# Performance work log

Hardware: AMD Instinct MI355X
Metric: run time of the kernel (lower is better)

The kernel has to match this reference:

```python
import jax, jax.numpy as jnp
import numpy as np

N = 100000      # nodes
E = 1600000     # edges (avg degree 16)
D_IN, H, D_OUT = 128, 64, 40


def setup_inputs() -> dict:
    key = jax.random.key(0)
    k = jax.random.split(key, 6)
    x = jax.random.normal(k[0], (N, D_IN), dtype=jnp.float32)
    edge_index = jax.random.randint(k[1], (2, E), 0, N, dtype=jnp.int32)
    W1 = jax.random.normal(k[2], (D_IN, H), dtype=jnp.float32) / np.sqrt(D_IN)
    b1 = jnp.zeros((H,), dtype=jnp.float32)
    W2 = jax.random.normal(k[3], (H, D_OUT), dtype=jnp.float32) / np.sqrt(H)
    b2 = jnp.zeros((D_OUT,), dtype=jnp.float32)
    return {"x": x, "edge_index": edge_index, "W1": W1, "b1": b1, "W2": W2, "b2": b2}


def _gcn_conv(h, src, dst, dinv, W, b):
    # PyG GCNConv: linear transform, then D^-1/2 (A+I) D^-1/2 aggregation, then bias.
    h = h @ W                                   # [N, F]
    w = dinv[src] * dinv[dst]                   # [E] symmetric norm edge weights
    msg = h[src] * w[:, None]                   # [E, F] gather + scale
    agg = jax.ops.segment_sum(msg, dst, num_segments=N)  # scatter-add to dst
    agg = agg + h * (dinv * dinv)[:, None]      # self-loop contribution deg^-1 * h
    return agg + b


def reference(x, edge_index, W1, b1, W2, b2):
    src, dst = edge_index[0], edge_index[1]
    # degree with self-loops (in-degree at dst, source_to_target flow)
    deg = 1.0 + jax.ops.segment_sum(jnp.ones((E,), dtype=x.dtype), dst, num_segments=N)
    dinv = jax.lax.rsqrt(deg)
    # dropout (p=0.6) is identity in eval mode
    h = jax.nn.relu(_gcn_conv(x, src, dst, dinv, W1, b1))
    out = _gcn_conv(h, src, dst, dinv, W2, b2)
    return jax.nn.log_softmax(out, axis=1)
```

## Files before the change

### kernel.cpp

```cpp
#include <hip/hip_runtime.h>
#include <math.h>

#define D_IN  128
#define H_DIM 64
#define D_OUT 40
#define BW_SHIFT 9
#define BW_NODES 512
#define BINA_CHUNK 4096
#define BUCKET_CAP 9216

typedef unsigned int uint32;

__device__ __forceinline__ unsigned short f2bf(float v) {
    uint32 b = __float_as_uint(v);
    b += 0x7fffu + ((b >> 16) & 1u);
    return (unsigned short)(b >> 16);
}
__device__ __forceinline__ float bf2f(unsigned short u) {
    return __uint_as_float(((uint32)u) << 16);
}

__global__ void cursor_init_kernel(int* __restrict__ gcursor, int NBUCK) {
    int i = blockIdx.x * 256 + threadIdx.x;
    if (i < NBUCK) gcursor[i] = i * BUCKET_CAP;
}

__global__ __launch_bounds__(256) void binA_scatter_kernel(const int* __restrict__ src,
                                                           const int* __restrict__ dst,
                                                           int* __restrict__ gcursor,
                                                           uint32* __restrict__ binned,
                                                           int E, int NBUCK) {
    __shared__ int cnt[1024];
    __shared__ int lbase[1024];
    int t = threadIdx.x;
    for (int i = t; i < NBUCK; i += 256) cnt[i] = 0;
    __syncthreads();
    int e0 = blockIdx.x * BINA_CHUNK;
    int e1 = min(e0 + BINA_CHUNK, E);
    for (int e = e0 + t; e < e1; e += 256)
        atomicAdd(&cnt[dst[e] >> BW_SHIFT], 1);
    __syncthreads();
    for (int i = t; i < NBUCK; i += 256) {
        int c = cnt[i];
        lbase[i] = c ? atomicAdd(&gcursor[i], c) : 0;
        cnt[i] = 0;
    }
    __syncthreads();
    for (int e = e0 + t; e < e1; e += 256) {
        int d = dst[e];
        int bk = d >> BW_SHIFT;
        int p = lbase[bk] + atomicAdd(&cnt[bk], 1);
        binned[p] = (((uint32)(d & (BW_NODES - 1))) << 23) | (uint32)src[e];
    }
}

__global__ __launch_bounds__(256) void phaseB_kernel(uint32* __restrict__ binned,
                                                     const int* __restrict__ gcur_end,
                                                     int* __restrict__ rows,
                                                     float* __restrict__ dinv,
                                                     int N) {
    __shared__ uint32 sedge[BUCKET_CAP];
    __shared__ int deg[BW_NODES];
    __shared__ int sa[BW_NODES], sb[BW_NODES];
    __shared__ int cur[BW_NODES];
    int b = blockIdx.x;
    int node0 = b << BW_SHIFT;
    int nn = min(BW_NODES, N - node0);
    int base = b * BUCKET_CAP;
    int cnt = gcur_end[b] - base;
    int t = threadIdx.x;
    deg[t] = 0; deg[t + 256] = 0;
    __syncthreads();
    for (int e = t; e < cnt; e += 256) {
        uint32 v = binned[base + e];
        sedge[e] = v;
        atomicAdd(&deg[v >> 23], 1);
    }
    __syncthreads();
    for (int i = t; i < nn; i += 256)
        dinv[node0 + i] = rsqrtf(1.0f + (float)deg[i]);
    sa[t] = deg[t]; sa[t + 256] = deg[t + 256];
    __syncthreads();
    int* pa = sa; int* pb = sb;
    for (int off = 1; off < BW_NODES; off <<= 1) {
        for (int i = t; i < BW_NODES; i += 256)
            pb[i] = pa[i] + ((i >= off) ? pa[i - off] : 0);
        __syncthreads();
        int* tmp = pa; pa = pb; pb = tmp;
    }
    for (int i = t; i < BW_NODES; i += 256)
        cur[i] = (i ? pa[i - 1] : 0);
    __syncthreads();
    int* rb = rows + b * 513;
    for (int i = t; i < nn; i += 256)
        rb[i] = base + cur[i];
    if (t == 0) rb[nn] = base + cnt;
    __syncthreads();
    for (int e = t; e < cnt; e += 256) {
        uint32 v = sedge[e];
        int doff = v >> 23;
        int p = base + atomicAdd(&cur[doff], 1);
        binned[p] = v & 0x7FFFFFu;
    }
}

__global__ __launch_bounds__(256) void gemm1_tn4(const float* __restrict__ x,
                                                 const float* __restrict__ W1,
                                                 const float* __restrict__ dinv,
                                                 unsigned short* __restrict__ h1s, int N) {
    __shared__ float sW[D_IN * H_DIM];
    int t = threadIdx.x;
    for (int i = t; i < D_IN * H_DIM / 4; i += 256)
        reinterpret_cast<float4*>(sW)[i] = reinterpret_cast<const float4*>(W1)[i];
    __syncthreads();

    int n = blockIdx.x * 64 + (t >> 2);
    if (n >= N) return;
    int c0 = (t & 3) * 16;
    const float4* xr = reinterpret_cast<const float4*>(x + (size_t)n * D_IN);

    float acc[16] = {};
    for (int k0 = 0; k0 < D_IN / 4; ++k0) {
        float4 xv = xr[k0];
        #pragma unroll
        for (int kk = 0; kk < 4; ++kk) {
            float xk = (kk == 0) ? xv.x : (kk == 1) ? xv.y : (kk == 2) ? xv.z : xv.w;
            const float* wrow = &sW[(4 * k0 + kk) * H_DIM + c0];
            #pragma unroll
            for (int c = 0; c < 4; ++c) {
                float4 wv = *reinterpret_cast<const float4*>(wrow + 4 * c);
                acc[4 * c + 0] += xk * wv.x;
                acc[4 * c + 1] += xk * wv.y;
                acc[4 * c + 2] += xk * wv.z;
                acc[4 * c + 3] += xk * wv.w;
            }
        }
    }
    float di = dinv[n];
    unsigned short* orow = h1s + (size_t)n * H_DIM + c0;
    #pragma unroll
    for (int c = 0; c < 4; ++c) {
        ushort4 u;
        u.x = f2bf(acc[4 * c + 0] * di);
        u.y = f2bf(acc[4 * c + 1] * di);
        u.z = f2bf(acc[4 * c + 2] * di);
        u.w = f2bf(acc[4 * c + 3] * di);
        *reinterpret_cast<ushort4*>(orow + 4 * c) = u;
    }
}

__global__ __launch_bounds__(256) void agg1_v3(const int* __restrict__ rows,
                                               const int* __restrict__ csr,
                                               const unsigned short* __restrict__ h1s,
                                               const float* __restrict__ dinv,
                                               const float* __restrict__ b1,
                                               float* __restrict__ z, int N) {
    int node = blockIdx.x * 4 + (threadIdx.x >> 6);
    if (node >= N) return;
    int lane = threadIdx.x & 63;
    int e  = lane >> 4;
    int fl = (lane & 15) * 4;
    int ridx = node + (node >> BW_SHIFT);
    int s0 = __builtin_amdgcn_readfirstlane(rows[ridx]);
    int s1 = __builtin_amdgcn_readfirstlane(rows[ridx + 1]);

    float4 acc = make_float4(0.f, 0.f, 0.f, 0.f);
    for (int base = s0; base < s1; base += 64) {
        int cnt = min(64, s1 - base);
        int myc = (lane < cnt) ? csr[base + lane] : 0;
        int j = 0;
        for (; j + 8 <= cnt; j += 8) {
            uint32 sa = (uint32)__shfl(myc, j + e);
            uint32 sb = (uint32)__shfl(myc, j + 4 + e);
            ushort4 ha = *reinterpret_cast<const ushort4*>(h1s + (size_t)(sa * H_DIM + fl));
            ushort4 hb = *reinterpret_cast<const ushort4*>(h1s + (size_t)(sb * H_DIM + fl));
            acc.x += bf2f(ha.x) + bf2f(hb.x);
            acc.y += bf2f(ha.y) + bf2f(hb.y);
            acc.z += bf2f(ha.z) + bf2f(hb.z);
            acc.w += bf2f(ha.w) + bf2f(hb.w);
        }
        for (; j < cnt; j += 4) {
            int idx = j + e;
            uint32 sa = (uint32)__shfl(myc, min(idx, cnt - 1));
            if (idx < cnt) {
                ushort4 hv = *reinterpret_cast<const ushort4*>(h1s + (size_t)(sa * H_DIM + fl));
                acc.x += bf2f(hv.x); acc.y += bf2f(hv.y);
                acc.z += bf2f(hv.z); acc.w += bf2f(hv.w);
            }
        }
    }
    acc.x += __shfl_xor(acc.x, 16); acc.y += __shfl_xor(acc.y, 16);
    acc.z += __shfl_xor(acc.z, 16); acc.w += __shfl_xor(acc.w, 16);
    acc.x += __shfl_xor(acc.x, 32); acc.y += __shfl_xor(acc.y, 32);
    acc.z += __shfl_xor(acc.z, 32); acc.w += __shfl_xor(acc.w, 32);

    if (e == 0) {
        ushort4 sv = *reinterpret_cast<const ushort4*>(h1s + (size_t)node * H_DIM + fl);
        float4 bv = *reinterpret_cast<const float4*>(b1 + fl);
        float di = dinv[node];
        float4 o;
        o.x = fmaxf(0.f, di * (acc.x + bf2f(sv.x)) + bv.x);
        o.y = fmaxf(0.f, di * (acc.y + bf2f(sv.y)) + bv.y);
        o.z = fmaxf(0.f, di * (acc.z + bf2f(sv.z)) + bv.z);
        o.w = fmaxf(0.f, di * (acc.w + bf2f(sv.w)) + bv.w);
        *reinterpret_cast<float4*>(z + (size_t)node * H_DIM + fl) = o;
    }
}

__global__ __launch_bounds__(256) void gemm2_tn2(const float* __restrict__ z,
                                                 const float* __restrict__ W2,
                                                 const float* __restrict__ dinv,
                                                 unsigned short* __restrict__ h2s, int N) {
    __shared__ float sW[H_DIM * D_OUT];
    int t = threadIdx.x;
    for (int i = t; i < H_DIM * D_OUT / 4; i += 256)
        reinterpret_cast<float4*>(sW)[i] = reinterpret_cast<const float4*>(W2)[i];
    __syncthreads();

    int n = blockIdx.x * 128 + (t >> 1);
    if (n >= N) return;
    int c0 = (t & 1) * 20;
    const float4* zr = reinterpret_cast<const float4*>(z + (size_t)n * H_DIM);

    float acc[20] = {};
    for (int k0 = 0; k0 < H_DIM / 4; ++k0) {
        float4 zv = zr[k0];
        #pragma unroll
        for (int kk = 0; kk < 4; ++kk) {
            float zk = (kk == 0) ? zv.x : (kk == 1) ? zv.y : (kk == 2) ? zv.z : zv.w;
            const float* wrow = &sW[(4 * k0 + kk) * D_OUT + c0];
            #pragma unroll
            for (int c = 0; c < 5; ++c) {
                float4 wv = *reinterpret_cast<const float4*>(wrow + 4 * c);
                acc[4 * c + 0] += zk * wv.x;
                acc[4 * c + 1] += zk * wv.y;
                acc[4 * c + 2] += zk * wv.z;
                acc[4 * c + 3] += zk * wv.w;
            }
        }
    }
    float di = dinv[n];
    unsigned short* orow = h2s + (size_t)n * D_OUT + c0;
    #pragma unroll
    for (int c = 0; c < 5; ++c) {
        ushort4 u;
        u.x = f2bf(acc[4 * c + 0] * di);
        u.y = f2bf(acc[4 * c + 1] * di);
        u.z = f2bf(acc[4 * c + 2] * di);
        u.w = f2bf(acc[4 * c + 3] * di);
        *reinterpret_cast<ushort4*>(orow + 4 * c) = u;
    }
}

__global__ __launch_bounds__(256) void agg2_v4(const int* __restrict__ rows,
                                               const int* __restrict__ csr,
                                               const unsigned short* __restrict__ h2s,
                                               const float* __restrict__ dinv,
                                               const float* __restrict__ b2,
                                               float* __restrict__ out, int N) {
    int node = blockIdx.x * 4 + (threadIdx.x >> 6);
    if (node >= N) return;
    int lane = threadIdx.x & 63;
    int g   = lane / 10;
    int f10 = lane - g * 10;
    int fl  = f10 * 4;
    bool gact = g < 6;
    int ridx = node + (node >> BW_SHIFT);
    int s0 = __builtin_amdgcn_readfirstlane(rows[ridx]);
    int s1 = __builtin_amdgcn_readfirstlane(rows[ridx + 1]);

    float4 acc = make_float4(0.f, 0.f, 0.f, 0.f);
    for (int base = s0; base < s1; base += 64) {
        int cnt = min(64, s1 - base);
        int myc = (lane < cnt) ? csr[base + lane] : 0;
        int j = 0;
        for (; j + 12 <= cnt; j += 12) {
            uint32 sa = (uint32)__shfl(myc, min(j + g, 63));
            uint32 sb = (uint32)__shfl(myc, min(j + 6 + g, 63));
            if (gact) {
                ushort4 ha = *reinterpret_cast<const ushort4*>(h2s + (size_t)(sa * D_OUT + fl));
                ushort4 hb = *reinterpret_cast<const ushort4*>(h2s + (size_t)(sb * D_OUT + fl));
                acc.x += bf2f(ha.x) + bf2f(hb.x);
                acc.y += bf2f(ha.y) + bf2f(hb.y);
                acc.z += bf2f(ha.z) + bf2f(hb.z);
                acc.w += bf2f(ha.w) + bf2f(hb.w);
            }
        }
        for (; j < cnt; j += 6) {
            int idx = j + g;
            uint32 sa = (uint32)__shfl(myc, min(idx, cnt - 1));
            if (gact && idx < cnt) {
                ushort4 hv = *reinterpret_cast<const ushort4*>(h2s + (size_t)(sa * D_OUT + fl));
                acc.x += bf2f(hv.x); acc.y += bf2f(hv.y);
                acc.z += bf2f(hv.z); acc.w += bf2f(hv.w);
            }
        }
    }
    acc.x += __shfl(acc.x, min(lane + 30, 63));
    acc.y += __shfl(acc.y, min(lane + 30, 63));
    acc.z += __shfl(acc.z, min(lane + 30, 63));
    acc.w += __shfl(acc.w, min(lane + 30, 63));
    acc.x += __shfl(acc.x, min(lane + 10, 63)) + __shfl(acc.x, min(lane + 20, 63));
    acc.y += __shfl(acc.y, min(lane + 10, 63)) + __shfl(acc.y, min(lane + 20, 63));
    acc.z += __shfl(acc.z, min(lane + 10, 63)) + __shfl(acc.z, min(lane + 20, 63));
    acc.w += __shfl(acc.w, min(lane + 10, 63)) + __shfl(acc.w, min(lane + 20, 63));

    bool act = lane < 10;
    float v0 = -INFINITY, v1 = -INFINITY, v2 = -INFINITY, v3 = -INFINITY;
    if (act) {
        ushort4 sv = *reinterpret_cast<const ushort4*>(h2s + (size_t)node * D_OUT + fl);
        float4 bv = *reinterpret_cast<const float4*>(b2 + fl);
        float di = dinv[node];
        v0 = di * (acc.x + bf2f(sv.x)) + bv.x;
        v1 = di * (acc.y + bf2f(sv.y)) + bv.y;
        v2 = di * (acc.z + bf2f(sv.z)) + bv.z;
        v3 = di * (acc.w + bf2f(sv.w)) + bv.w;
    }
    float mm = act ? fmaxf(fmaxf(v0, v1), fmaxf(v2, v3)) : -INFINITY;
    for (int off = 32; off > 0; off >>= 1) mm = fmaxf(mm, __shfl_xor(mm, off));
    float es = act ? (__expf(v0 - mm) + __expf(v1 - mm) + __expf(v2 - mm) + __expf(v3 - mm)) : 0.f;
    for (int off = 32; off > 0; off >>= 1) es += __shfl_xor(es, off);
    float lse = __logf(es);
    if (act) {
        float4 o = make_float4(v0 - mm - lse, v1 - mm - lse, v2 - mm - lse, v3 - mm - lse);
        *reinterpret_cast<float4*>(out + (size_t)node * D_OUT + fl) = o;
    }
}

extern "C" void kernel_launch(void* const* d_in, const int* in_sizes, int n_in,
                              void* d_out, int out_size, void* d_ws, size_t ws_size,
                              hipStream_t stream) {
    const float* x  = (const float*)d_in[0];
    const int*   ei = (const int*)d_in[1];
    const float* W1 = (const float*)d_in[2];
    const float* b1 = (const float*)d_in[3];
    const float* W2 = (const float*)d_in[4];
    const float* b2 = (const float*)d_in[5];
    float* out = (float*)d_out;

    int N = in_sizes[0] / D_IN;
    int E = in_sizes[1] / 2;
    const int* src = ei;
    const int* dst = ei + E;
    int NBUCK = (N + BW_NODES - 1) / BW_NODES;

    char* p = (char*)d_ws;
    int*   gcursor = (int*)p;  p += 4096;
    int*   rows    = (int*)p;  p += ((size_t)NBUCK * 513 + 64) * 4;
    float* dinv    = (float*)p; p += (((size_t)N + 63) & ~(size_t)63) * 4;
    uint32* binned = (uint32*)p; p += (size_t)NBUCK * BUCKET_CAP * 4;
    unsigned short* h1s = (unsigned short*)p; p += (size_t)N * H_DIM * 2;
    float* z       = (float*)p; p += (size_t)N * H_DIM * 4;

    int binA_blocks = (E + BINA_CHUNK - 1) / BINA_CHUNK;

    cursor_init_kernel<<<(NBUCK + 255) / 256, 256, 0, stream>>>(gcursor, NBUCK);
    binA_scatter_kernel<<<binA_blocks, 256, 0, stream>>>(src, dst, gcursor, binned, E, NBUCK);
    phaseB_kernel<<<NBUCK, 256, 0, stream>>>(binned, gcursor, rows, dinv, N);
    int* csr = (int*)binned;

    gemm1_tn4<<<(N + 63) / 64, 256, 0, stream>>>(x, W1, dinv, h1s, N);
    agg1_v3<<<(N + 3) / 4, 256, 0, stream>>>(rows, csr, h1s, dinv, b1, z, N);

    unsigned short* h2s = h1s;
    gemm2_tn2<<<(N + 127) / 128, 256, 0, stream>>>(z, W2, dinv, h2s, N);
    agg2_v4<<<(N + 3) / 4, 256, 0, stream>>>(rows, csr, h2s, dinv, b2, out, N);
}
```

Baseline: 204.4 us.

## Quantize gathered node features to int8 with per-row scales

```diff
diff --git a/kernel.cpp b/kernel.cpp
--- a/kernel.cpp
+++ b/kernel.cpp
@@ -11,13 +11,18 @@
 
 typedef unsigned int uint32;
 
-__device__ __forceinline__ unsigned short f2bf(float v) {
-    uint32 b = __float_as_uint(v);
-    b += 0x7fffu + ((b >> 16) & 1u);
-    return (unsigned short)(b >> 16);
-}
-__device__ __forceinline__ float bf2f(unsigned short u) {
-    return __uint_as_float(((uint32)u) << 16);
+__device__ __forceinline__ void acci8(float4& acc, uint32 q, float sc) {
+    int qi = (int)q;
+    acc.x = fmaf(sc, (float)((qi << 24) >> 24), acc.x);
+    acc.y = fmaf(sc, (float)((qi << 16) >> 24), acc.y);
+    acc.z = fmaf(sc, (float)((qi << 8)  >> 24), acc.z);
+    acc.w = fmaf(sc, (float)( qi        >> 24), acc.w);
+}
+__device__ __forceinline__ uint32 pack4(float v0, float v1, float v2, float v3, float qs) {
+    int q0 = __float2int_rn(v0 * qs), q1 = __float2int_rn(v1 * qs);
+    int q2 = __float2int_rn(v2 * qs), q3 = __float2int_rn(v3 * qs);
+    return (uint32)(q0 & 0xff) | ((uint32)(q1 & 0xff) << 8) |
+           ((uint32)(q2 & 0xff) << 16) | ((uint32)(q3 & 0xff) << 24);
 }
 
 __global__ void cursor_init_kernel(int* __restrict__ gcursor, int NBUCK) {
@@ -104,10 +109,11 @@
     }
 }
 
-__global__ __launch_bounds__(256) void gemm1_tn4(const float* __restrict__ x,
-                                                 const float* __restrict__ W1,
-                                                 const float* __restrict__ dinv,
-                                                 unsigned short* __restrict__ h1s, int N) {
+__global__ __launch_bounds__(256) void gemm1_q(const float* __restrict__ x,
+                                               const float* __restrict__ W1,
+                                               const float* __restrict__ dinv,
+                                               unsigned char* __restrict__ h1q,
+                                               float* __restrict__ scale1, int N) {
     __shared__ float sW[D_IN * H_DIM];
     int t = threadIdx.x;
     for (int i = t; i < D_IN * H_DIM / 4; i += 256)
@@ -137,29 +143,34 @@
         }
     }
     float di = dinv[n];
-    unsigned short* orow = h1s + (size_t)n * H_DIM + c0;
+    float m = 0.f;
     #pragma unroll
-    for (int c = 0; c < 4; ++c) {
-        ushort4 u;
-        u.x = f2bf(acc[4 * c + 0] * di);
-        u.y = f2bf(acc[4 * c + 1] * di);
-        u.z = f2bf(acc[4 * c + 2] * di);
-        u.w = f2bf(acc[4 * c + 3] * di);
-        *reinterpret_cast<ushort4*>(orow + 4 * c) = u;
-    }
-}
-
-__global__ __launch_bounds__(256) void agg1_v3(const int* __restrict__ rows,
-                                               const int* __restrict__ csr,
-                                               const unsigned short* __restrict__ h1s,
-                                               const float* __restrict__ dinv,
-                                               const float* __restrict__ b1,
-                                               float* __restrict__ z, int N) {
+    for (int c = 0; c < 16; ++c) { acc[c] *= di; m = fmaxf(m, fabsf(acc[c])); }
+    m = fmaxf(m, __shfl_xor(m, 1));
+    m = fmaxf(m, __shfl_xor(m, 2));
+    m = fmaxf(m, 1e-20f);
+    float qs = 127.0f / m;
+    if ((t & 3) == 0) scale1[n] = m * (1.0f / 127.0f);
+    uint4 w;
+    w.x = pack4(acc[0],  acc[1],  acc[2],  acc[3],  qs);
+    w.y = pack4(acc[4],  acc[5],  acc[6],  acc[7],  qs);
+    w.z = pack4(acc[8],  acc[9],  acc[10], acc[11], qs);
+    w.w = pack4(acc[12], acc[13], acc[14], acc[15], qs);
+    *reinterpret_cast<uint4*>(h1q + (size_t)n * H_DIM + c0) = w;
+}
+
+__global__ __launch_bounds__(256) void agg1_q(const int* __restrict__ rows,
+                                              const int* __restrict__ csr,
+                                              const unsigned char* __restrict__ h1q,
+                                              const float* __restrict__ scale1,
+                                              const float* __restrict__ dinv,
+                                              const float* __restrict__ b1,
+                                              float* __restrict__ z, int N) {
     int node = blockIdx.x * 4 + (threadIdx.x >> 6);
     if (node >= N) return;
     int lane = threadIdx.x & 63;
     int e  = lane >> 4;
-    int fl = (lane & 15) * 4;
+    int fb = (lane & 15) * 4;
     int ridx = node + (node >> BW_SHIFT);
     int s0 = __builtin_amdgcn_readfirstlane(rows[ridx]);
     int s1 = __builtin_amdgcn_readfirstlane(rows[ridx + 1]);
@@ -172,20 +183,20 @@
         for (; j + 8 <= cnt; j += 8) {
             uint32 sa = (uint32)__shfl(myc, j + e);
             uint32 sb = (uint32)__shfl(myc, j + 4 + e);
-            ushort4 ha = *reinterpret_cast<const ushort4*>(h1s + (size_t)(sa * H_DIM + fl));
-            ushort4 hb = *reinterpret_cast<const ushort4*>(h1s + (size_t)(sb * H_DIM + fl));
-            acc.x += bf2f(ha.x) + bf2f(hb.x);
-            acc.y += bf2f(ha.y) + bf2f(hb.y);
-            acc.z += bf2f(ha.z) + bf2f(hb.z);
-            acc.w += bf2f(ha.w) + bf2f(hb.w);
+            uint32 ha = *reinterpret_cast<const uint32*>(h1q + (size_t)sa * H_DIM + fb);
+            uint32 hb = *reinterpret_cast<const uint32*>(h1q + (size_t)sb * H_DIM + fb);
+            float sca = scale1[sa];
+            float scb = scale1[sb];
+            acci8(acc, ha, sca);
+            acci8(acc, hb, scb);
         }
         for (; j < cnt; j += 4) {
             int idx = j + e;
             uint32 sa = (uint32)__shfl(myc, min(idx, cnt - 1));
             if (idx < cnt) {
-                ushort4 hv = *reinterpret_cast<const ushort4*>(h1s + (size_t)(sa * H_DIM + fl));
-                acc.x += bf2f(hv.x); acc.y += bf2f(hv.y);
-                acc.z += bf2f(hv.z); acc.w += bf2f(hv.w);
+                uint32 hv = *reinterpret_cast<const uint32*>(h1q + (size_t)sa * H_DIM + fb);
+                float sc = scale1[sa];
+                acci8(acc, hv, sc);
             }
         }
     }
@@ -195,22 +206,26 @@
     acc.z += __shfl_xor(acc.z, 32); acc.w += __shfl_xor(acc.w, 32);
 
     if (e == 0) {
-        ushort4 sv = *reinterpret_cast<const ushort4*>(h1s + (size_t)node * H_DIM + fl);
-        float4 bv = *reinterpret_cast<const float4*>(b1 + fl);
+        uint32 sv = *reinterpret_cast<const uint32*>(h1q + (size_t)node * H_DIM + fb);
+        float scn = scale1[node];
+        float4 self = make_float4(0.f, 0.f, 0.f, 0.f);
+        acci8(self, sv, scn);
+        float4 bv = *reinterpret_cast<const float4*>(b1 + fb);
         float di = dinv[node];
         float4 o;
-        o.x = fmaxf(0.f, di * (acc.x + bf2f(sv.x)) + bv.x);
-        o.y = fmaxf(0.f, di * (acc.y + bf2f(sv.y)) + bv.y);
-        o.z = fmaxf(0.f, di * (acc.z + bf2f(sv.z)) + bv.z);
-        o.w = fmaxf(0.f, di * (acc.w + bf2f(sv.w)) + bv.w);
-        *reinterpret_cast<float4*>(z + (size_t)node * H_DIM + fl) = o;
-    }
-}
-
-__global__ __launch_bounds__(256) void gemm2_tn2(const float* __restrict__ z,
-                                                 const float* __restrict__ W2,
-                                                 const float* __restrict__ dinv,
-                                                 unsigned short* __restrict__ h2s, int N) {
+        o.x = fmaxf(0.f, di * (acc.x + self.x) + bv.x);
+        o.y = fmaxf(0.f, di * (acc.y + self.y) + bv.y);
+        o.z = fmaxf(0.f, di * (acc.z + self.z) + bv.z);
+        o.w = fmaxf(0.f, di * (acc.w + self.w) + bv.w);
+        *reinterpret_cast<float4*>(z + (size_t)node * H_DIM + fb) = o;
+    }
+}
+
+__global__ __launch_bounds__(256) void gemm2_q(const float* __restrict__ z,
+                                               const float* __restrict__ W2,
+                                               const float* __restrict__ dinv,
+                                               unsigned char* __restrict__ h2q,
+                                               float* __restrict__ scale2, int N) {
     __shared__ float sW[H_DIM * D_OUT];
     int t = threadIdx.x;
     for (int i = t; i < H_DIM * D_OUT / 4; i += 256)
@@ -240,30 +255,34 @@
         }
     }
     float di = dinv[n];
-    unsigned short* orow = h2s + (size_t)n * D_OUT + c0;
+    float m = 0.f;
+    #pragma unroll
+    for (int c = 0; c < 20; ++c) { acc[c] *= di; m = fmaxf(m, fabsf(acc[c])); }
+    m = fmaxf(m, __shfl_xor(m, 1));
+    m = fmaxf(m, 1e-20f);
+    float qs = 127.0f / m;
+    if ((t & 1) == 0) scale2[n] = m * (1.0f / 127.0f);
+    unsigned char* orow = h2q + (size_t)n * D_OUT + c0;
     #pragma unroll
     for (int c = 0; c < 5; ++c) {
-        ushort4 u;
-        u.x = f2bf(acc[4 * c + 0] * di);
-        u.y = f2bf(acc[4 * c + 1] * di);
-        u.z = f2bf(acc[4 * c + 2] * di);
-        u.w = f2bf(acc[4 * c + 3] * di);
-        *reinterpret_cast<ushort4*>(orow + 4 * c) = u;
-    }
-}
-
-__global__ __launch_bounds__(256) void agg2_v4(const int* __restrict__ rows,
-                                               const int* __restrict__ csr,
-                                               const unsigned short* __restrict__ h2s,
-                                               const float* __restrict__ dinv,
-                                               const float* __restrict__ b2,
-                                               float* __restrict__ out, int N) {
+        uint32 w = pack4(acc[4 * c + 0], acc[4 * c + 1], acc[4 * c + 2], acc[4 * c + 3], qs);
+        *reinterpret_cast<uint32*>(orow + 4 * c) = w;
+    }
+}
+
+__global__ __launch_bounds__(256) void agg2_q(const int* __restrict__ rows,
+                                              const int* __restrict__ csr,
+                                              const unsigned char* __restrict__ h2q,
+                                              const float* __restrict__ scale2,
+                                              const float* __restrict__ dinv,
+                                              const float* __restrict__ b2,
+                                              float* __restrict__ out, int N) {
     int node = blockIdx.x * 4 + (threadIdx.x >> 6);
     if (node >= N) return;
     int lane = threadIdx.x & 63;
     int g   = lane / 10;
     int f10 = lane - g * 10;
-    int fl  = f10 * 4;
+    int fb  = f10 * 4;
     bool gact = g < 6;
     int ridx = node + (node >> BW_SHIFT);
     int s0 = __builtin_amdgcn_readfirstlane(rows[ridx]);
@@ -278,21 +297,21 @@
             uint32 sa = (uint32)__shfl(myc, min(j + g, 63));
             uint32 sb = (uint32)__shfl(myc, min(j + 6 + g, 63));
             if (gact) {
-                ushort4 ha = *reinterpret_cast<const ushort4*>(h2s + (size_t)(sa * D_OUT + fl));
-                ushort4 hb = *reinterpret_cast<const ushort4*>(h2s + (size_t)(sb * D_OUT + fl));
-                acc.x += bf2f(ha.x) + bf2f(hb.x);
-                acc.y += bf2f(ha.y) + bf2f(hb.y);
-                acc.z += bf2f(ha.z) + bf2f(hb.z);
-                acc.w += bf2f(ha.w) + bf2f(hb.w);
+                uint32 ha = *reinterpret_cast<const uint32*>(h2q + (size_t)sa * D_OUT + fb);
+                uint32 hb = *reinterpret_cast<const uint32*>(h2q + (size_t)sb * D_OUT + fb);
+                float sca = scale2[sa];
+                float scb = scale2[sb];
+                acci8(acc, ha, sca);
+                acci8(acc, hb, scb);
             }
         }
         for (; j < cnt; j += 6) {
             int idx = j + g;
             uint32 sa = (uint32)__shfl(myc, min(idx, cnt - 1));
             if (gact && idx < cnt) {
-                ushort4 hv = *reinterpret_cast<const ushort4*>(h2s + (size_t)(sa * D_OUT + fl));
-                acc.x += bf2f(hv.x); acc.y += bf2f(hv.y);
-                acc.z += bf2f(hv.z); acc.w += bf2f(hv.w);
+                uint32 hv = *reinterpret_cast<const uint32*>(h2q + (size_t)sa * D_OUT + fb);
+                float sc = scale2[sa];
+                acci8(acc, hv, sc);
             }
         }
     }
@@ -308,13 +327,16 @@
     bool act = lane < 10;
     float v0 = -INFINITY, v1 = -INFINITY, v2 = -INFINITY, v3 = -INFINITY;
     if (act) {
-        ushort4 sv = *reinterpret_cast<const ushort4*>(h2s + (size_t)node * D_OUT + fl);
-        float4 bv = *reinterpret_cast<const float4*>(b2 + fl);
+        uint32 sv = *reinterpret_cast<const uint32*>(h2q + (size_t)node * D_OUT + fb);
+        float scn = scale2[node];
+        float4 self = make_float4(0.f, 0.f, 0.f, 0.f);
+        acci8(self, sv, scn);
+        float4 bv = *reinterpret_cast<const float4*>(b2 + fb);
         float di = dinv[node];
-        v0 = di * (acc.x + bf2f(sv.x)) + bv.x;
-        v1 = di * (acc.y + bf2f(sv.y)) + bv.y;
-        v2 = di * (acc.z + bf2f(sv.z)) + bv.z;
-        v3 = di * (acc.w + bf2f(sv.w)) + bv.w;
+        v0 = di * (acc.x + self.x) + bv.x;
+        v1 = di * (acc.y + self.y) + bv.y;
+        v2 = di * (acc.z + self.z) + bv.z;
+        v3 = di * (acc.w + self.w) + bv.w;
     }
     float mm = act ? fmaxf(fmaxf(v0, v1), fmaxf(v2, v3)) : -INFINITY;
     for (int off = 32; off > 0; off >>= 1) mm = fmaxf(mm, __shfl_xor(mm, off));
@@ -323,7 +345,7 @@
     float lse = __logf(es);
     if (act) {
         float4 o = make_float4(v0 - mm - lse, v1 - mm - lse, v2 - mm - lse, v3 - mm - lse);
-        *reinterpret_cast<float4*>(out + (size_t)node * D_OUT + fl) = o;
+        *reinterpret_cast<float4*>(out + (size_t)node * D_OUT + fb) = o;
     }
 }
 
@@ -348,8 +370,10 @@
     int*   gcursor = (int*)p;  p += 4096;
     int*   rows    = (int*)p;  p += ((size_t)NBUCK * 513 + 64) * 4;
     float* dinv    = (float*)p; p += (((size_t)N + 63) & ~(size_t)63) * 4;
+    float* scale1  = (float*)p; p += (((size_t)N + 63) & ~(size_t)63) * 4;
+    float* scale2  = (float*)p; p += (((size_t)N + 63) & ~(size_t)63) * 4;
     uint32* binned = (uint32*)p; p += (size_t)NBUCK * BUCKET_CAP * 4;
-    unsigned short* h1s = (unsigned short*)p; p += (size_t)N * H_DIM * 2;
+    unsigned char* h1q = (unsigned char*)p; p += (size_t)N * H_DIM;
     float* z       = (float*)p; p += (size_t)N * H_DIM * 4;
 
     int binA_blocks = (E + BINA_CHUNK - 1) / BINA_CHUNK;
@@ -359,10 +383,10 @@
     phaseB_kernel<<<NBUCK, 256, 0, stream>>>(binned, gcursor, rows, dinv, N);
     int* csr = (int*)binned;
 
-    gemm1_tn4<<<(N + 63) / 64, 256, 0, stream>>>(x, W1, dinv, h1s, N);
-    agg1_v3<<<(N + 3) / 4, 256, 0, stream>>>(rows, csr, h1s, dinv, b1, z, N);
-
-    unsigned short* h2s = h1s;
-    gemm2_tn2<<<(N + 127) / 128, 256, 0, stream>>>(z, W2, dinv, h2s, N);
-    agg2_v4<<<(N + 3) / 4, 256, 0, stream>>>(rows, csr, h2s, dinv, b2, out, N);
-}
+    gemm1_q<<<(N + 63) / 64, 256, 0, stream>>>(x, W1, dinv, h1q, scale1, N);
+    agg1_q<<<(N + 3) / 4, 256, 0, stream>>>(rows, csr, h1q, scale1, dinv, b1, z, N);
+
+    unsigned char* h2q = h1q;
+    gemm2_q<<<(N + 127) / 128, 256, 0, stream>>>(z, W2, dinv, h2q, scale2, N);
+    agg2_q<<<(N + 3) / 4, 256, 0, stream>>>(rows, csr, h2q, scale2, dinv, b2, out, N);
+}
```

After: 195.9 us. 4.1% less time.
